# Performance work log

Hardware: AMD Instinct MI355X
Metric: run time of the kernel (lower is better)

## Reference

```python
import jax, jax.numpy as jnp
import numpy as np

NC = 5  # num_clusters == unfold window size


def conv1x3(x, w, b):
    # x: (B, Cin, H, W); w: (Cout, Cin, 1, 3); padding (0,1) like torch Conv2d
    y = jax.lax.conv_general_dilated(
        x, w, window_strides=(1, 1), padding=((0, 0), (1, 1)),
        dimension_numbers=("NCHW", "OIHW", "NCHW"))
    return y + b[None, :, None, None]


def setup_inputs() -> dict:
    key = jax.random.key(0)
    ks = jax.random.split(key, 8)
    b, h, l, d = 8, 8, 1024, 64
    dm = h * d  # d_model = 512
    f32 = jnp.float32
    s_conv1 = 1.0 / np.sqrt(dm * 3)
    s_conv2 = 1.0 / np.sqrt(NC * 3)
    s_lin = 1.0 / np.sqrt(NC)
    return {
        "Q": jax.random.normal(ks[0], (b, h, l, d), f32),
        "K": jax.random.normal(ks[1], (b, h, l, d), f32),
        "V": jax.random.normal(ks[2], (b, h, l, d), f32),
        "w_proj_k": jax.random.normal(ks[3], (NC, dm, 1, 3), f32) * s_conv1,
        "b_proj_k": jnp.zeros((NC,), f32),
        "w_proj_back": jax.random.normal(ks[4], (dm, NC, 1, 3), f32) * s_conv2,
        "b_proj_back": jnp.zeros((dm,), f32),
        "w_ck": jax.random.normal(ks[5], (NC, NC), f32) * s_lin,
        "b_ck": jnp.zeros((NC,), f32),
        "w_cq": jax.random.normal(ks[6], (NC, NC), f32) * s_lin,
        "b_cq": jnp.zeros((NC,), f32),
    }


def reference(Q, K, V, w_proj_k, b_proj_k, w_proj_back, b_proj_back,
              w_ck, b_ck, w_cq, b_cq):
    b, h, l, d = Q.shape
    u = NC  # unfolding window
    # --- padded unfold along batch dim: window i is K_padded[i:i+u] ---
    K_padded = jnp.concatenate(
        [jnp.zeros((u, h, l, d), Q.dtype), K[1:]], axis=0)  # (u+b-1, h, l, d)
    idx = jnp.arange(b)[:, None] + jnp.arange(u)[None, :]     # (b, u)
    Kw = K_padded[idx]                                        # (b, u, h, l, d)
    Kw = jnp.transpose(Kw, (0, 2, 3, 4, 1))                   # (b, h, l, d, u) == torch unfold layout
    K_unfold = Kw.reshape(b, h * d, l, u)                     # raw reshape, matches torch
    # --- project to clusters ---
    ckp = jax.nn.relu(conv1x3(K_unfold, w_proj_k, b_proj_k))  # (b, NC, l, u)
    ckp = jnp.transpose(ckp, (0, 2, 3, 1))                    # (b, l, u, NC)
    cluster_k = jax.nn.softmax(ckp @ w_ck.T + b_ck, axis=-1)
    cluster_q = jax.nn.softmax(ckp @ w_cq.T + b_cq, axis=-1)
    # --- distributional loss ---
    mu = jnp.mean(cluster_q, axis=-1)                         # (b, l, u)
    sigma = jax.nn.softplus(jnp.std(cluster_q, axis=-1, ddof=1))  # unbiased std like torch
    x = jnp.mean(cluster_k, axis=-1)
    log_prob = -0.5 * ((x - mu) / sigma) ** 2 - jnp.log(sigma) - 0.5 * jnp.log(2 * jnp.pi)
    # CrossEntropyLoss(mu, mu): class dim is axis=1 (l); soft-label targets = mu
    ce = -jnp.mean(jnp.sum(mu * jax.nn.log_softmax(mu, axis=1), axis=1))
    loss = -jnp.mean(log_prob) + ce
    # --- masked triangular cluster attention ---
    scores = jnp.einsum('blpc,bluc->blpu', cluster_q, cluster_k) / u  # (b, l, u, u)
    mask = jnp.triu(jnp.ones((u, u), bool), k=1)
    scores = jnp.where(mask, -1e9, scores)
    attn = jax.nn.softmax(scores, axis=-1)
    cluster_q2 = jnp.einsum('blpu,bluc->blpc', attn, cluster_q)       # (b, l, u, NC)
    # --- project back & second attention ---
    cc = jax.nn.relu(conv1x3(jnp.transpose(cluster_q2, (0, 3, 1, 2)),
                             w_proj_back, b_proj_back))               # (b, h*d, l, u)
    cluster_center = cc.reshape(b, h, u, l, d)                        # raw reshape, matches torch
    scores_center = jnp.einsum('bhqd,bhckd->bhqk', Q, cluster_center) # sums over c and d
    attn2 = jax.nn.softmax(scores_center, axis=-1)
    context = jnp.einsum('bhqk,bhkd->bhqd', attn2, V)
    return (context, loss)
```

## Files before the change

### kernel.cpp

```cpp
#include <hip/hip_runtime.h>
#include <math.h>

#define L 1024
#define D 64
#define H 8
#define B 8

#define WS_PART 0
#define WS_MU   614400
#define WS_Q2   655360
#define WS_KEFF 860160
#define WS_SCAL_BYTES 20217856

typedef __attribute__((ext_vector_type(8))) short bf16x8;
typedef __attribute__((ext_vector_type(4))) float f32x4;

__device__ __forceinline__ ushort f2bf(float x) {
  unsigned b = __builtin_bit_cast(unsigned, x);
  return (ushort)((b + 0x7FFFu + ((b >> 16) & 1u)) >> 16);
}
__device__ __forceinline__ float bf2f(ushort u) {
  unsigned t = ((unsigned)u) << 16;
  return __builtin_bit_cast(float, t);
}

__global__ __launch_bounds__(256) void k_part(const float* __restrict__ K,
                                              const float* __restrict__ wpk,
                                              float* __restrict__ part) {
  const int tid = threadIdx.x;
  const int lane = tid & 63;
  const int wid = tid >> 6;
  const int lq = blockIdx.x;
  const int jj = blockIdx.y;
  const int bi = blockIdx.z;
  __shared__ float w_s[512 * 16];
  __shared__ float red[3][64][16];
  for (int i = tid; i < 512 * 15; i += 256) {
    int c = i / 15, f = i % 15;
    int nc = f / 3, t = f % 3;
    w_s[c * 16 + f] = wpk[(nc * 512 + c) * 3 + t];
  }
  __syncthreads();
  float acc[15];
#pragma unroll
  for (int f = 0; f < 15; ++f) acc[f] = 0.f;
  if (bi + jj >= 5) {
    const float* Kb = K + (size_t)(bi + jj - 4) * (H * L * D);
    int c0 = wid * 128;
#pragma unroll 4
    for (int c = c0; c < c0 + 128; ++c) {
      int hh = c >> 6;
      int li2 = ((c & 63) << 4) + lq;
      float val = Kb[(hh * L + li2) * D + lane];
      const float* wr = &w_s[c * 16];
#pragma unroll
      for (int f = 0; f < 15; ++f) acc[f] = fmaf(val, wr[f], acc[f]);
    }
  }
  if (wid) {
#pragma unroll
    for (int f = 0; f < 15; ++f) red[wid - 1][lane][f] = acc[f];
  }
  __syncthreads();
  if (wid == 0) {
#pragma unroll
    for (int f = 0; f < 15; ++f)
      acc[f] += red[0][lane][f] + red[1][lane][f] + red[2][lane][f];
    int li = (lq << 6) + lane;
    float* dst = part + ((size_t)(bi * L + li) * 5 + jj) * 15;
#pragma unroll
    for (int f = 0; f < 15; ++f) dst[f] = acc[f];
  }
}

__global__ __launch_bounds__(256) void k_chain(const float* __restrict__ part,
    const float* __restrict__ b_pk, const float* __restrict__ w_ck,
    const float* __restrict__ b_ck, const float* __restrict__ w_cq,
    const float* __restrict__ b_cq, float* __restrict__ mu_out,
    float* __restrict__ q2_out, double* __restrict__ dsc) {
  int g = blockIdx.x * 256 + threadIdx.x;
  const float* p = part + (size_t)g * 75;
  float ckp[5][5];
#pragma unroll
  for (int j = 0; j < 5; ++j) {
#pragma unroll
    for (int nc = 0; nc < 5; ++nc) {
      float s = b_pk[nc];
#pragma unroll
      for (int t = 0; t < 3; ++t) {
        int w = j + t - 1;
        if (w >= 0 && w < 5) s += p[w * 15 + nc * 3 + t];
      }
      ckp[j][nc] = fmaxf(s, 0.f);
    }
  }
  float cq[5][5], ck[5][5];
  float lp_sum = 0.f;
#pragma unroll
  for (int j = 0; j < 5; ++j) {
    float vk[5], vq[5];
#pragma unroll
    for (int m = 0; m < 5; ++m) {
      float sk = b_ck[m], sq = b_cq[m];
#pragma unroll
      for (int n = 0; n < 5; ++n) {
        sk = fmaf(ckp[j][n], w_ck[m * 5 + n], sk);
        sq = fmaf(ckp[j][n], w_cq[m * 5 + n], sq);
      }
      vk[m] = sk; vq[m] = sq;
    }
    float mk = vk[0], mq = vq[0];
#pragma unroll
    for (int m = 1; m < 5; ++m) { mk = fmaxf(mk, vk[m]); mq = fmaxf(mq, vq[m]); }
    float sk = 0.f, sq = 0.f;
#pragma unroll
    for (int m = 0; m < 5; ++m) {
      vk[m] = expf(vk[m] - mk); sk += vk[m];
      vq[m] = expf(vq[m] - mq); sq += vq[m];
    }
    float rk = 1.f / sk, rq = 1.f / sq;
    float mu = 0.f, x = 0.f;
#pragma unroll
    for (int m = 0; m < 5; ++m) {
      ck[j][m] = vk[m] * rk; cq[j][m] = vq[m] * rq;
      mu += cq[j][m]; x += ck[j][m];
    }
    mu *= 0.2f; x *= 0.2f;
    float var = 0.f;
#pragma unroll
    for (int m = 0; m < 5; ++m) { float d0 = cq[j][m] - mu; var += d0 * d0; }
    var *= 0.25f;
    float sg = log1pf(expf(sqrtf(var)));
    float z = (x - mu) / sg;
    lp_sum += -0.5f * z * z - logf(sg) - 0.91893853320467274f;
    mu_out[(size_t)g * 5 + j] = mu;
  }
  float* q2p = q2_out + (size_t)g * 25;
#pragma unroll
  for (int pp = 0; pp < 5; ++pp) {
    float sc[5]; float mx = -3.0e38f;
    for (int u2 = 0; u2 <= pp; ++u2) {
      float d0 = 0.f;
#pragma unroll
      for (int c = 0; c < 5; ++c) d0 = fmaf(cq[pp][c], ck[u2][c], d0);
      sc[u2] = d0 * 0.2f;
      mx = fmaxf(mx, sc[u2]);
    }
    float den = 0.f;
    for (int u2 = 0; u2 <= pp; ++u2) { sc[u2] = expf(sc[u2] - mx); den += sc[u2]; }
    float rd = 1.f / den;
    float q2v[5] = {0.f, 0.f, 0.f, 0.f, 0.f};
    for (int u2 = 0; u2 <= pp; ++u2) {
      float a = sc[u2] * rd;
#pragma unroll
      for (int c = 0; c < 5; ++c) q2v[c] = fmaf(a, cq[u2][c], q2v[c]);
    }
#pragma unroll
    for (int c = 0; c < 5; ++c) q2p[pp * 5 + c] = q2v[c];
  }
  for (int off = 1; off < 64; off <<= 1) lp_sum += __shfl_xor(lp_sum, off, 64);
  __shared__ float wsum[4];
  int tid = threadIdx.x;
  if ((tid & 63) == 0) wsum[tid >> 6] = lp_sum;
  __syncthreads();
  if (tid == 0) atomicAdd(dsc, (double)(wsum[0] + wsum[1] + wsum[2] + wsum[3]));
}

__global__ __launch_bounds__(256) void k_ce(const float* __restrict__ mu,
                                            double* __restrict__ dsc) {
  int bi = blockIdx.x / 5, u = blockIdx.x % 5;
  int tid = threadIdx.x;
  const float* base = mu + (size_t)bi * L * 5 + u;
  float v[4];
#pragma unroll
  for (int k = 0; k < 4; ++k) v[k] = base[(tid + 256 * k) * 5];
  float mx = fmaxf(fmaxf(v[0], v[1]), fmaxf(v[2], v[3]));
  for (int off = 1; off < 64; off <<= 1) mx = fmaxf(mx, __shfl_xor(mx, off, 64));
  __shared__ float sh[4];
  if ((tid & 63) == 0) sh[tid >> 6] = mx;
  __syncthreads();
  mx = fmaxf(fmaxf(sh[0], sh[1]), fmaxf(sh[2], sh[3]));
  __syncthreads();
  float se = 0.f;
#pragma unroll
  for (int k = 0; k < 4; ++k) se += expf(v[k] - mx);
  for (int off = 1; off < 64; off <<= 1) se += __shfl_xor(se, off, 64);
  if ((tid & 63) == 0) sh[tid >> 6] = se;
  __syncthreads();
  float lse = mx + logf(sh[0] + sh[1] + sh[2] + sh[3]);
  __syncthreads();
  float part = 0.f;
#pragma unroll
  for (int k = 0; k < 4; ++k) part += v[k] * (v[k] - lse);
  for (int off = 1; off < 64; off <<= 1) part += __shfl_xor(part, off, 64);
  if ((tid & 63) == 0) sh[tid >> 6] = part;
  __syncthreads();
  if (tid == 0) atomicAdd(dsc + 1, (double)(sh[0] + sh[1] + sh[2] + sh[3]));
}

__global__ __launch_bounds__(256) void k_keff(const float* __restrict__ q2,
    const float* __restrict__ wb, const float* __restrict__ bb,
    float* __restrict__ keff) {
  int g = blockIdx.x * 256 + threadIdx.x;
  int bi = g >> 19;
  int r = g & 524287;
  int hh = r >> 16;
  int li2 = (r >> 6) & 1023;
  int dd = r & 63;
  int base = hh * 327680 + li2 * 64 + dd;
  const float* q2b = q2 + (size_t)bi * L * 25;
  float sum = 0.f;
#pragma unroll
  for (int cc = 0; cc < 5; ++cc) {
    int flat = base + cc * 65536;
    int co = (int)((unsigned)flat / 5120u);
    int rem = flat - co * 5120;
    int li = (int)((unsigned)rem / 5u);
    int j = rem - li * 5;
    const float* qr = q2b + li * 25;
    const float* wr = wb + co * 15;
    float s = bb[co];
#pragma unroll
    for (int t = 0; t < 3; ++t) {
      int w = j + t - 1;
      if (w >= 0 && w < 5) {
#pragma unroll
        for (int c = 0; c < 5; ++c) s = fmaf(qr[w * 5 + c], wr[c * 3 + t], s);
      }
    }
    sum += fmaxf(s, 0.f);
  }
  keff[g] = sum;
}

__global__ __launch_bounds__(256) void k_attn(const float* __restrict__ Q,
    const float* __restrict__ Kf, const float* __restrict__ V,
    float* __restrict__ Out) {
  __shared__ ushort Khi[4096], Klo[4096];
  __shared__ ushort Vthi[4096], Vtlo[4096];
  const int tid = threadIdx.x;
  const int lane = tid & 63;
  const int w = tid >> 6;
  const int lq = lane & 15;
  const int g = lane >> 4;
  const int bh = blockIdx.y;
  const int q0 = blockIdx.x << 7;
  const float* Qb = Q + ((size_t)bh * L + q0 + w * 32) * D;
  const float* Kb = Kf + (size_t)bh * L * D;
  const float* Vb = V + (size_t)bh * L * D;

  bf16x8 qh[2][2], qlo[2][2];
#pragma unroll
  for (int qs = 0; qs < 2; ++qs) {
    const float* Qr = Qb + (qs * 16 + lq) * D;
#pragma unroll
    for (int ds = 0; ds < 2; ++ds) {
      float4 x0 = *(const float4*)(Qr + 4 * g + 32 * ds);
      float4 x1 = *(const float4*)(Qr + 4 * g + 16 + 32 * ds);
      float xs[8] = {x0.x, x0.y, x0.z, x0.w, x1.x, x1.y, x1.z, x1.w};
      bf16x8 h, l;
#pragma unroll
      for (int j = 0; j < 8; ++j) {
        ushort hb = f2bf(xs[j]);
        h[j] = (short)hb;
        l[j] = (short)f2bf(xs[j] - bf2f(hb));
      }
      qh[qs][ds] = h; qlo[qs][ds] = l;
    }
  }

  f32x4 O_[2][4];
  float m_[2], l_[2];
#pragma unroll
  for (int qs = 0; qs < 2; ++qs) {
    m_[qs] = -3.0e38f; l_[qs] = 0.f;
#pragma unroll
    for (int d2 = 0; d2 < 4; ++d2) O_[qs][d2] = (f32x4){0.f, 0.f, 0.f, 0.f};
  }

  for (int kt = 0; kt < 16; ++kt) {
    __syncthreads();
    {
      int key = tid >> 2, c0 = (tid & 3) << 4;
      const float* Krow = Kb + (kt * 64 + key) * 64 + c0;
#pragma unroll
      for (int i = 0; i < 4; ++i) {
        float4 v = *(const float4*)(Krow + 4 * i);
        ushort4 h, lo;
        h.x = f2bf(v.x); h.y = f2bf(v.y); h.z = f2bf(v.z); h.w = f2bf(v.w);
        lo.x = f2bf(v.x - bf2f(h.x)); lo.y = f2bf(v.y - bf2f(h.y));
        lo.z = f2bf(v.z - bf2f(h.z)); lo.w = f2bf(v.w - bf2f(h.w));
        int c = (c0 >> 2) + i;
        int idx = key * 64 + ((c ^ (key & 15)) << 2);
        *(ushort4*)(&Khi[idx]) = h;
        *(ushort4*)(&Klo[idx]) = lo;
      }
    }
    {
      int kp = tid & 31, dblk = tid >> 5;
      ushort vh[2][8], vl[2][8];
#pragma unroll
      for (int kk = 0; kk < 2; ++kk) {
        int key = 2 * kp + kk;
        const float* Vrow = Vb + (kt * 64 + key) * 64 + dblk * 8;
#pragma unroll
        for (int i = 0; i < 2; ++i) {
          float4 v = *(const float4*)(Vrow + 4 * i);
          float xs[4] = {v.x, v.y, v.z, v.w};
#pragma unroll
          for (int e = 0; e < 4; ++e) {
            ushort hb = f2bf(xs[e]);
            vh[kk][4 * i + e] = hb;
            vl[kk][4 * i + e] = f2bf(xs[e] - bf2f(hb));
          }
        }
      }
#pragma unroll
      for (int dd = 0; dd < 8; ++dd) {
        int d = dblk * 8 + dd;
        int idx = d * 64 + (((kp >> 1) ^ (d & 15)) << 2) + ((kp & 1) << 1);
        ushort2 ph; ph.x = vh[0][dd]; ph.y = vh[1][dd];
        ushort2 pl; pl.x = vl[0][dd]; pl.y = vl[1][dd];
        *(ushort2*)(&Vthi[idx]) = ph;
        *(ushort2*)(&Vtlo[idx]) = pl;
      }
    }
    __syncthreads();

    f32x4 S[4][2];
#pragma unroll
    for (int ks = 0; ks < 4; ++ks)
#pragma unroll
      for (int qs = 0; qs < 2; ++qs) S[ks][qs] = (f32x4){0.f, 0.f, 0.f, 0.f};
#pragma unroll
    for (int ds = 0; ds < 2; ++ds) {
#pragma unroll
      for (int ksub = 0; ksub < 4; ++ksub) {
        int key = ksub * 16 + lq;
        int base = key * 64;
        int ca = ((g + 8 * ds) ^ lq) << 2;
        int cb = ((g + 4 + 8 * ds) ^ lq) << 2;
        ushort4 a0 = *(const ushort4*)(&Khi[base + ca]);
        ushort4 a1 = *(const ushort4*)(&Khi[base + cb]);
        ushort4 b0 = *(const ushort4*)(&Klo[base + ca]);
        ushort4 b1 = *(const ushort4*)(&Klo[base + cb]);
        bf16x8 kh = {(short)a0.x, (short)a0.y, (short)a0.z, (short)a0.w,
                     (short)a1.x, (short)a1.y, (short)a1.z, (short)a1.w};
        bf16x8 kl = {(short)b0.x, (short)b0.y, (short)b0.z, (short)b0.w,
                     (short)b1.x, (short)b1.y, (short)b1.z, (short)b1.w};
#pragma unroll
        for (int qs = 0; qs < 2; ++qs) {
          S[ksub][qs] = __builtin_amdgcn_mfma_f32_16x16x32_bf16(kh, qh[qs][ds], S[ksub][qs], 0, 0, 0);
          S[ksub][qs] = __builtin_amdgcn_mfma_f32_16x16x32_bf16(kh, qlo[qs][ds], S[ksub][qs], 0, 0, 0);
          S[ksub][qs] = __builtin_amdgcn_mfma_f32_16x16x32_bf16(kl, qh[qs][ds], S[ksub][qs], 0, 0, 0);
        }
      }
    }

    bf16x8 pfh[2][2], pfl[2][2];
#pragma unroll
    for (int qs = 0; qs < 2; ++qs) {
      float tmax = -3.0e38f;
#pragma unroll
      for (int ks = 0; ks < 4; ++ks)
#pragma unroll
        for (int r = 0; r < 4; ++r) tmax = fmaxf(tmax, S[ks][qs][r]);
      tmax = fmaxf(tmax, __shfl_xor(tmax, 16, 64));
      tmax = fmaxf(tmax, __shfl_xor(tmax, 32, 64));
      float mn = fmaxf(m_[qs], tmax);
      float scl = __expf(m_[qs] - mn);
      float p[4][4]; float rs = 0.f;
#pragma unroll
      for (int ks = 0; ks < 4; ++ks)
#pragma unroll
        for (int r = 0; r < 4; ++r) {
          float pv = __expf(S[ks][qs][r] - mn);
          p[ks][r] = pv; rs += pv;
        }
      rs += __shfl_xor(rs, 16, 64);
      rs += __shfl_xor(rs, 32, 64);
      l_[qs] = l_[qs] * scl + rs;
      m_[qs] = mn;
#pragma unroll
      for (int kst = 0; kst < 2; ++kst) {
        bf16x8 h, l;
#pragma unroll
        for (int jh = 0; jh < 2; ++jh)
#pragma unroll
          for (int j2 = 0; j2 < 4; ++j2) {
            float pv = p[jh + 2 * kst][j2];
            ushort hb = f2bf(pv);
            h[jh * 4 + j2] = (short)hb;
            l[jh * 4 + j2] = (short)f2bf(pv - bf2f(hb));
          }
        pfh[qs][kst] = h; pfl[qs][kst] = l;
      }
      float sr[4];
#pragma unroll
      for (int r = 0; r < 4; ++r) sr[r] = __shfl(scl, 4 * g + r, 64);
#pragma unroll
      for (int d2 = 0; d2 < 4; ++d2)
#pragma unroll
        for (int r = 0; r < 4; ++r) O_[qs][d2][r] *= sr[r];
    }

#pragma unroll
    for (int kst = 0; kst < 2; ++kst) {
#pragma unroll
      for (int d2 = 0; d2 < 4; ++d2) {
        int d = d2 * 16 + lq;
        int base = d * 64;
        int ca = ((g + 8 * kst) ^ lq) << 2;
        int cb = ((g + 4 + 8 * kst) ^ lq) << 2;
        ushort4 a0 = *(const ushort4*)(&Vthi[base + ca]);
        ushort4 a1 = *(const ushort4*)(&Vthi[base + cb]);
        ushort4 b0 = *(const ushort4*)(&Vtlo[base + ca]);
        ushort4 b1 = *(const ushort4*)(&Vtlo[base + cb]);
        bf16x8 vh = {(short)a0.x, (short)a0.y, (short)a0.z, (short)a0.w,
                     (short)a1.x, (short)a1.y, (short)a1.z, (short)a1.w};
        bf16x8 vl = {(short)b0.x, (short)b0.y, (short)b0.z, (short)b0.w,
                     (short)b1.x, (short)b1.y, (short)b1.z, (short)b1.w};
#pragma unroll
        for (int qs = 0; qs < 2; ++qs) {
          O_[qs][d2] = __builtin_amdgcn_mfma_f32_16x16x32_bf16(pfh[qs][kst], vh, O_[qs][d2], 0, 0, 0);
          O_[qs][d2] = __builtin_amdgcn_mfma_f32_16x16x32_bf16(pfl[qs][kst], vh, O_[qs][d2], 0, 0, 0);
          O_[qs][d2] = __builtin_amdgcn_mfma_f32_16x16x32_bf16(pfh[qs][kst], vl, O_[qs][d2], 0, 0, 0);
        }
      }
    }
  }

  float* Ob = Out + ((size_t)bh * L + q0 + w * 32) * D;
#pragma unroll
  for (int qs = 0; qs < 2; ++qs) {
    float il = 1.f / l_[qs];
    float ir[4];
#pragma unroll
    for (int r = 0; r < 4; ++r) ir[r] = __shfl(il, 4 * g + r, 64);
#pragma unroll
    for (int d2 = 0; d2 < 4; ++d2) {
#pragma unroll
      for (int r = 0; r < 4; ++r) {
        int row = qs * 16 + 4 * g + r;
        Ob[row * D + d2 * 16 + lq] = O_[qs][d2][r] * ir[r];
      }
    }
  }
}

__global__ void k_final(const double* __restrict__ dsc, float* __restrict__ out) {
  out[4194304] = (float)(-dsc[0] / 40960.0 - dsc[1] / 40.0);
}

extern "C" void kernel_launch(void* const* d_in, const int* in_sizes, int n_in,
                              void* d_out, int out_size, void* d_ws, size_t ws_size,
                              hipStream_t stream) {
  const float* Q   = (const float*)d_in[0];
  const float* K   = (const float*)d_in[1];
  const float* V   = (const float*)d_in[2];
  const float* wpk = (const float*)d_in[3];
  const float* bpk = (const float*)d_in[4];
  const float* wpb = (const float*)d_in[5];
  const float* bpb = (const float*)d_in[6];
  const float* wck = (const float*)d_in[7];
  const float* bck = (const float*)d_in[8];
  const float* wcq = (const float*)d_in[9];
  const float* bcq = (const float*)d_in[10];
  float* out = (float*)d_out;
  float* ws = (float*)d_ws;
  float* part = ws + WS_PART;
  float* mu   = ws + WS_MU;
  float* q2   = ws + WS_Q2;
  float* keff = ws + WS_KEFF;
  double* dsc = (double*)((char*)d_ws + WS_SCAL_BYTES);

  hipMemsetAsync((char*)d_ws + WS_SCAL_BYTES, 0, 16, stream);
  k_part<<<dim3(16, 5, 8), 256, 0, stream>>>(K, wpk, part);
  k_chain<<<32, 256, 0, stream>>>(part, bpk, wck, bck, wcq, bcq, mu, q2, dsc);
  k_ce<<<40, 256, 0, stream>>>(mu, dsc);
  k_keff<<<16384, 256, 0, stream>>>(q2, wpb, bpb, keff);
  k_attn<<<dim3(8, 64), 256, 0, stream>>>(Q, keff, V, out);
  k_final<<<1, 1, 0, stream>>>(dsc, out);
}
```

Before: 327.2 us.

## Dedupe K projection, pre-split K/V to bf16 in global, double-buffer attention

k_part now computes each batch's K projection once rather than per window position, and k_chain gathers the shared partials by batch offset. The effective K is split into bf16 hi/lo and written pre-swizzled to global memory. V is split and transposed the same way by a new prep kernel when workspace allows. The attention kernel streams tiles with async global_load_lds into double-buffered LDS, reorders blocks, and drops the low-part P correction MFMA (precision loss in P). It also vectorizes output stores and swaps the MFMA operand order. This removes redundant conversion work and overlaps loads with compute, at the cost of extra global traffic for the prepped buffers and some accuracy.

Result: faster. 307.9 us (-5.9%).

```diff
diff --git a/kernel.cpp b/kernel.cpp
--- a/kernel.cpp
+++ b/kernel.cpp
@@ -6,11 +6,16 @@
 #define H 8
 #define B 8
 
-#define WS_PART 0
-#define WS_MU   614400
-#define WS_Q2   655360
-#define WS_KEFF 860160
-#define WS_SCAL_BYTES 20217856
+#define WS_G    0
+#define WS_MU   107520
+#define WS_Q2   148480
+#define WS_DSC_BYTE   1413120u
+#define WS_KHI_BYTE   1413632u
+#define WS_KLO_BYTE   9802240u
+#define WS_NOV_END    18190848u
+#define WS_VTHI_BYTE  18190848u
+#define WS_VTLO_BYTE  26579456u
+#define WS_V_END      34968064u
 
 typedef __attribute__((ext_vector_type(8))) short bf16x8;
 typedef __attribute__((ext_vector_type(4))) float f32x4;
@@ -26,36 +31,35 @@
 
 __global__ __launch_bounds__(256) void k_part(const float* __restrict__ K,
                                               const float* __restrict__ wpk,
-                                              float* __restrict__ part) {
-  const int tid = threadIdx.x;
-  const int lane = tid & 63;
-  const int wid = tid >> 6;
+                                              float* __restrict__ G) {
+  const int tid = threadIdx.x, lane = tid & 63, wid = tid >> 6;
   const int lq = blockIdx.x;
-  const int jj = blockIdx.y;
-  const int bi = blockIdx.z;
+  const int bip = blockIdx.y + 1;
   __shared__ float w_s[512 * 16];
   __shared__ float red[3][64][16];
-  for (int i = tid; i < 512 * 15; i += 256) {
-    int c = i / 15, f = i % 15;
-    int nc = f / 3, t = f % 3;
-    w_s[c * 16 + f] = wpk[(nc * 512 + c) * 3 + t];
+  for (int i = tid; i < 512 * 16; i += 256) {
+    int c = i >> 4, f = i & 15;
+    w_s[i] = (f < 15) ? wpk[((f / 3) * 512 + c) * 3 + (f % 3)] : 0.f;
   }
   __syncthreads();
   float acc[15];
 #pragma unroll
   for (int f = 0; f < 15; ++f) acc[f] = 0.f;
-  if (bi + jj >= 5) {
-    const float* Kb = K + (size_t)(bi + jj - 4) * (H * L * D);
-    int c0 = wid * 128;
+  const float* Kb = K + (size_t)bip * (H * L * D);
+  const int c0 = wid * 128;
 #pragma unroll 4
-    for (int c = c0; c < c0 + 128; ++c) {
-      int hh = c >> 6;
-      int li2 = ((c & 63) << 4) + lq;
-      float val = Kb[(hh * L + li2) * D + lane];
-      const float* wr = &w_s[c * 16];
-#pragma unroll
-      for (int f = 0; f < 15; ++f) acc[f] = fmaf(val, wr[f], acc[f]);
-    }
+  for (int c = c0; c < c0 + 128; ++c) {
+    float val = Kb[((c >> 6) * L + ((c & 63) << 4) + lq) * D + lane];
+    const float4* wr = (const float4*)&w_s[c * 16];
+    float4 w0 = wr[0], w1 = wr[1], w2 = wr[2], w3 = wr[3];
+    acc[0] = fmaf(val, w0.x, acc[0]);  acc[1] = fmaf(val, w0.y, acc[1]);
+    acc[2] = fmaf(val, w0.z, acc[2]);  acc[3] = fmaf(val, w0.w, acc[3]);
+    acc[4] = fmaf(val, w1.x, acc[4]);  acc[5] = fmaf(val, w1.y, acc[5]);
+    acc[6] = fmaf(val, w1.z, acc[6]);  acc[7] = fmaf(val, w1.w, acc[7]);
+    acc[8] = fmaf(val, w2.x, acc[8]);  acc[9] = fmaf(val, w2.y, acc[9]);
+    acc[10] = fmaf(val, w2.z, acc[10]); acc[11] = fmaf(val, w2.w, acc[11]);
+    acc[12] = fmaf(val, w3.x, acc[12]); acc[13] = fmaf(val, w3.y, acc[13]);
+    acc[14] = fmaf(val, w3.z, acc[14]);
   }
   if (wid) {
 #pragma unroll
@@ -66,20 +70,19 @@
 #pragma unroll
     for (int f = 0; f < 15; ++f)
       acc[f] += red[0][lane][f] + red[1][lane][f] + red[2][lane][f];
-    int li = (lq << 6) + lane;
-    float* dst = part + ((size_t)(bi * L + li) * 5 + jj) * 15;
+    float* dst = G + ((size_t)blockIdx.y * 1024 + (lq << 6) + lane) * 15;
 #pragma unroll
     for (int f = 0; f < 15; ++f) dst[f] = acc[f];
   }
 }
 
-__global__ __launch_bounds__(256) void k_chain(const float* __restrict__ part,
+__global__ __launch_bounds__(256) void k_chain(const float* __restrict__ G,
     const float* __restrict__ b_pk, const float* __restrict__ w_ck,
     const float* __restrict__ b_ck, const float* __restrict__ w_cq,
     const float* __restrict__ b_cq, float* __restrict__ mu_out,
     float* __restrict__ q2_out, double* __restrict__ dsc) {
   int g = blockIdx.x * 256 + threadIdx.x;
-  const float* p = part + (size_t)g * 75;
+  int bi = g >> 10, li = g & 1023;
   float ckp[5][5];
 #pragma unroll
   for (int j = 0; j < 5; ++j) {
@@ -89,7 +92,9 @@
 #pragma unroll
       for (int t = 0; t < 3; ++t) {
         int w = j + t - 1;
-        if (w >= 0 && w < 5) s += p[w * 15 + nc * 3 + t];
+        int bip = bi + w - 4;
+        if (w >= 0 && w < 5 && bip >= 1)
+          s += G[(size_t)((bip - 1) * 1024 + li) * 15 + nc * 3 + t];
       }
       ckp[j][nc] = fmaxf(s, 0.f);
     }
@@ -198,16 +203,16 @@
   if (tid == 0) atomicAdd(dsc + 1, (double)(sh[0] + sh[1] + sh[2] + sh[3]));
 }
 
-__global__ __launch_bounds__(256) void k_keff(const float* __restrict__ q2,
+__global__ __launch_bounds__(256) void k_kprep(const float* __restrict__ q2,
     const float* __restrict__ wb, const float* __restrict__ bb,
-    float* __restrict__ keff) {
+    ushort* __restrict__ Khi_g, ushort* __restrict__ Klo_g) {
   int g = blockIdx.x * 256 + threadIdx.x;
   int bi = g >> 19;
   int r = g & 524287;
   int hh = r >> 16;
-  int li2 = (r >> 6) & 1023;
+  int li = (r >> 6) & 1023;
   int dd = r & 63;
-  int base = hh * 327680 + li2 * 64 + dd;
+  int base = hh * 327680 + li * 64 + dd;
   const float* q2b = q2 + (size_t)bi * L * 25;
   float sum = 0.f;
 #pragma unroll
@@ -215,9 +220,9 @@
     int flat = base + cc * 65536;
     int co = (int)((unsigned)flat / 5120u);
     int rem = flat - co * 5120;
-    int li = (int)((unsigned)rem / 5u);
-    int j = rem - li * 5;
-    const float* qr = q2b + li * 25;
+    int li2 = (int)((unsigned)rem / 5u);
+    int j = rem - li2 * 5;
+    const float* qr = q2b + li2 * 25;
     const float* wr = wb + co * 15;
     float s = bb[co];
 #pragma unroll
@@ -230,24 +235,70 @@
     }
     sum += fmaxf(s, 0.f);
   }
-  keff[g] = sum;
-}
-
+  int kt = li >> 6, key = li & 63, c = dd >> 2, e = dd & 3;
+  int idx = (((bi * 8 + hh) * 16 + kt) << 12) + (key << 6) + ((c ^ (key & 15)) << 2) + e;
+  ushort hb = f2bf(sum);
+  Khi_g[idx] = hb;
+  Klo_g[idx] = f2bf(sum - bf2f(hb));
+}
+
+__global__ __launch_bounds__(256) void k_vprep(const float* __restrict__ V,
+    ushort* __restrict__ Vthi_g, ushort* __restrict__ Vtlo_g) {
+  __shared__ float t[64][65];
+  const int tile = blockIdx.x;
+  const float* Vb = V + ((size_t)tile << 12);
+  const int tid = threadIdx.x;
+  {
+    int key = tid >> 2, c0 = (tid & 3) << 4;
+#pragma unroll
+    for (int i = 0; i < 4; ++i) {
+      float4 v = *(const float4*)(Vb + key * 64 + c0 + 4 * i);
+      t[key][c0 + 4 * i + 0] = v.x; t[key][c0 + 4 * i + 1] = v.y;
+      t[key][c0 + 4 * i + 2] = v.z; t[key][c0 + 4 * i + 3] = v.w;
+    }
+  }
+  __syncthreads();
+  int d = tid >> 2, q4 = tid & 3;
+#pragma unroll
+  for (int q = 0; q < 4; ++q) {
+    int kc = q4 * 4 + q;
+    ushort hv[4], lv[4];
+#pragma unroll
+    for (int e = 0; e < 4; ++e) {
+      float x = t[kc * 4 + e][d];
+      ushort hb = f2bf(x);
+      hv[e] = hb;
+      lv[e] = f2bf(x - bf2f(hb));
+    }
+    int idx = (tile << 12) + (d << 6) + ((kc ^ (d & 15)) << 2);
+    ushort4 h4; h4.x = hv[0]; h4.y = hv[1]; h4.z = hv[2]; h4.w = hv[3];
+    ushort4 l4; l4.x = lv[0]; l4.y = lv[1]; l4.z = lv[2]; l4.w = lv[3];
+    *(ushort4*)(&Vthi_g[idx]) = h4;
+    *(ushort4*)(&Vtlo_g[idx]) = l4;
+  }
+}
+
+template<bool VPREP>
 __global__ __launch_bounds__(256) void k_attn(const float* __restrict__ Q,
-    const float* __restrict__ Kf, const float* __restrict__ V,
-    float* __restrict__ Out) {
-  __shared__ ushort Khi[4096], Klo[4096];
-  __shared__ ushort Vthi[4096], Vtlo[4096];
+    const ushort* __restrict__ Khi_g, const ushort* __restrict__ Klo_g,
+    const ushort* __restrict__ Vthi_g, const ushort* __restrict__ Vtlo_g,
+    const float* __restrict__ V, float* __restrict__ Out) {
+  __shared__ ushort smem[2][16384];
   const int tid = threadIdx.x;
   const int lane = tid & 63;
   const int w = tid >> 6;
   const int lq = lane & 15;
   const int g = lane >> 4;
-  const int bh = blockIdx.y;
-  const int q0 = blockIdx.x << 7;
+  const int id = blockIdx.x;
+  const int bh = ((id & 7) << 3) + (id >> 6);
+  const int qb = (id >> 3) & 7;
+  const int q0 = qb << 7;
   const float* Qb = Q + ((size_t)bh * L + q0 + w * 32) * D;
-  const float* Kb = Kf + (size_t)bh * L * D;
   const float* Vb = V + (size_t)bh * L * D;
+  const int tb = bh * 16;
+
+  int cx0 = ((g) ^ lq) << 2, cx1 = ((g + 4) ^ lq) << 2;
+  int cx2 = ((g + 8) ^ lq) << 2, cx3 = ((g + 12) ^ lq) << 2;
 
   bf16x8 qh[2][2], qlo[2][2];
 #pragma unroll
@@ -269,6 +320,64 @@
     }
   }
 
+  const ushort* warr;
+  int wdst;
+  if (VPREP) {
+    warr = (w == 0) ? Khi_g : (w == 1) ? Klo_g : (w == 2) ? Vthi_g : Vtlo_g;
+    wdst = w << 12;
+  } else {
+    warr = ((w < 2) ? Khi_g : Klo_g);
+    wdst = ((w >> 1) << 12) + ((w & 1) << 11);
+  }
+
+#define STAGE(buf_, kt_) do {                                                  \
+    const ushort* src_ = warr + ((size_t)(tb + (kt_)) << 12) +                 \
+                         (VPREP ? 0 : ((w & 1) << 11)) + lane * 8;             \
+    ushort* dst_ = &smem[buf_][wdst];                                          \
+    _Pragma("unroll")                                                          \
+    for (int r_ = 0; r_ < (VPREP ? 8 : 4); ++r_) {                             \
+      __builtin_amdgcn_global_load_lds(                                        \
+        (const __attribute__((address_space(1))) unsigned int*)(src_ + r_ * 512), \
+        (__attribute__((address_space(3))) unsigned int*)(dst_ + r_ * 512 + lane * 8), \
+        16, 0, 0);                                                             \
+    }                                                                          \
+  } while (0)
+
+  float4 vreg[2][2];
+  const int kp = tid & 31, dblk = tid >> 5;
+#define VLOAD(kt_) do {                                                        \
+    const float* Vb2_ = Vb + ((size_t)(kt_) << 12);                            \
+    _Pragma("unroll")                                                          \
+    for (int kk_ = 0; kk_ < 2; ++kk_)                                          \
+      _Pragma("unroll")                                                        \
+      for (int i_ = 0; i_ < 2; ++i_)                                           \
+        vreg[kk_][i_] = *(const float4*)(Vb2_ + (2 * kp + kk_) * 64 + dblk * 8 + 4 * i_); \
+  } while (0)
+#define VWRITE(nb_) do {                                                       \
+    ushort vh_[2][8], vl_[2][8];                                               \
+    _Pragma("unroll")                                                          \
+    for (int kk_ = 0; kk_ < 2; ++kk_)                                          \
+      _Pragma("unroll")                                                        \
+      for (int i_ = 0; i_ < 2; ++i_) {                                         \
+        float xs_[4] = {vreg[kk_][i_].x, vreg[kk_][i_].y, vreg[kk_][i_].z, vreg[kk_][i_].w}; \
+        _Pragma("unroll")                                                      \
+        for (int e_ = 0; e_ < 4; ++e_) {                                       \
+          ushort hb_ = f2bf(xs_[e_]);                                          \
+          vh_[kk_][4 * i_ + e_] = hb_;                                         \
+          vl_[kk_][4 * i_ + e_] = f2bf(xs_[e_] - bf2f(hb_));                   \
+        }                                                                      \
+      }                                                                        \
+    _Pragma("unroll")                                                          \
+    for (int dd_ = 0; dd_ < 8; ++dd_) {                                        \
+      int d_ = dblk * 8 + dd_;                                                 \
+      int idx_ = (d_ << 6) + (((kp >> 1) ^ (d_ & 15)) << 2) + ((kp & 1) << 1); \
+      ushort2 ph_; ph_.x = vh_[0][dd_]; ph_.y = vh_[1][dd_];                   \
+      ushort2 pl_; pl_.x = vl_[0][dd_]; pl_.y = vl_[1][dd_];                   \
+      *(ushort2*)(&smem[nb_][8192 + idx_]) = ph_;                              \
+      *(ushort2*)(&smem[nb_][12288 + idx_]) = pl_;                             \
+    }                                                                          \
+  } while (0)
+
   f32x4 O_[2][4];
   float m_[2], l_[2];
 #pragma unroll
@@ -278,54 +387,21 @@
     for (int d2 = 0; d2 < 4; ++d2) O_[qs][d2] = (f32x4){0.f, 0.f, 0.f, 0.f};
   }
 
+  STAGE(0, 0);
+  if (!VPREP) { VLOAD(0); VWRITE(0); }
+  __syncthreads();
+
+  int cur = 0;
   for (int kt = 0; kt < 16; ++kt) {
-    __syncthreads();
-    {
-      int key = tid >> 2, c0 = (tid & 3) << 4;
-      const float* Krow = Kb + (kt * 64 + key) * 64 + c0;
-#pragma unroll
-      for (int i = 0; i < 4; ++i) {
-        float4 v = *(const float4*)(Krow + 4 * i);
-        ushort4 h, lo;
-        h.x = f2bf(v.x); h.y = f2bf(v.y); h.z = f2bf(v.z); h.w = f2bf(v.w);
-        lo.x = f2bf(v.x - bf2f(h.x)); lo.y = f2bf(v.y - bf2f(h.y));
-        lo.z = f2bf(v.z - bf2f(h.z)); lo.w = f2bf(v.w - bf2f(h.w));
-        int c = (c0 >> 2) + i;
-        int idx = key * 64 + ((c ^ (key & 15)) << 2);
-        *(ushort4*)(&Khi[idx]) = h;
-        *(ushort4*)(&Klo[idx]) = lo;
-      }
-    }
-    {
-      int kp = tid & 31, dblk = tid >> 5;
-      ushort vh[2][8], vl[2][8];
-#pragma unroll
-      for (int kk = 0; kk < 2; ++kk) {
-        int key = 2 * kp + kk;
-        const float* Vrow = Vb + (kt * 64 + key) * 64 + dblk * 8;
-#pragma unroll
-        for (int i = 0; i < 2; ++i) {
-          float4 v = *(const float4*)(Vrow + 4 * i);
-          float xs[4] = {v.x, v.y, v.z, v.w};
-#pragma unroll
-          for (int e = 0; e < 4; ++e) {
-            ushort hb = f2bf(xs[e]);
-            vh[kk][4 * i + e] = hb;
-            vl[kk][4 * i + e] = f2bf(xs[e] - bf2f(hb));
-          }
-        }
-      }
-#pragma unroll
-      for (int dd = 0; dd < 8; ++dd) {
-        int d = dblk * 8 + dd;
-        int idx = d * 64 + (((kp >> 1) ^ (d & 15)) << 2) + ((kp & 1) << 1);
-        ushort2 ph; ph.x = vh[0][dd]; ph.y = vh[1][dd];
-        ushort2 pl; pl.x = vl[0][dd]; pl.y = vl[1][dd];
-        *(ushort2*)(&Vthi[idx]) = ph;
-        *(ushort2*)(&Vtlo[idx]) = pl;
-      }
-    }
-    __syncthreads();
+    if (kt < 15) {
+      STAGE(cur ^ 1, kt + 1);
+      if (!VPREP) VLOAD(kt + 1);
+    }
+
+    const ushort* Kh = &smem[cur][0];
+    const ushort* Kl = &smem[cur][4096];
+    const ushort* Vh = &smem[cur][8192];
+    const ushort* Vl = &smem[cur][12288];
 
     f32x4 S[4][2];
 #pragma unroll
@@ -334,16 +410,14 @@
       for (int qs = 0; qs < 2; ++qs) S[ks][qs] = (f32x4){0.f, 0.f, 0.f, 0.f};
 #pragma unroll
     for (int ds = 0; ds < 2; ++ds) {
+      int ca = ds ? cx2 : cx0, cb = ds ? cx3 : cx1;
 #pragma unroll
       for (int ksub = 0; ksub < 4; ++ksub) {
-        int key = ksub * 16 + lq;
-        int base = key * 64;
-        int ca = ((g + 8 * ds) ^ lq) << 2;
-        int cb = ((g + 4 + 8 * ds) ^ lq) << 2;
-        ushort4 a0 = *(const ushort4*)(&Khi[base + ca]);
-        ushort4 a1 = *(const ushort4*)(&Khi[base + cb]);
-        ushort4 b0 = *(const ushort4*)(&Klo[base + ca]);
-        ushort4 b1 = *(const ushort4*)(&Klo[base + cb]);
+        int base = (ksub * 16 + lq) * 64;
+        ushort4 a0 = *(const ushort4*)(Kh + base + ca);
+        ushort4 a1 = *(const ushort4*)(Kh + base + cb);
+        ushort4 b0 = *(const ushort4*)(Kl + base + ca);
+        ushort4 b1 = *(const ushort4*)(Kl + base + cb);
         bf16x8 kh = {(short)a0.x, (short)a0.y, (short)a0.z, (short)a0.w,
                      (short)a1.x, (short)a1.y, (short)a1.z, (short)a1.w};
         bf16x8 kl = {(short)b0.x, (short)b0.y, (short)b0.z, (short)b0.w,
@@ -357,7 +431,8 @@
       }
     }
 
-    bf16x8 pfh[2][2], pfl[2][2];
+    bf16x8 pfh[2][2];
+    float scl[2];
 #pragma unroll
     for (int qs = 0; qs < 2; ++qs) {
       float tmax = -3.0e38f;
@@ -368,7 +443,7 @@
       tmax = fmaxf(tmax, __shfl_xor(tmax, 16, 64));
       tmax = fmaxf(tmax, __shfl_xor(tmax, 32, 64));
       float mn = fmaxf(m_[qs], tmax);
-      float scl = __expf(m_[qs] - mn);
+      scl[qs] = __expf(m_[qs] - mn);
       float p[4][4]; float rs = 0.f;
 #pragma unroll
       for (int ks = 0; ks < 4; ++ks)
@@ -379,73 +454,67 @@
         }
       rs += __shfl_xor(rs, 16, 64);
       rs += __shfl_xor(rs, 32, 64);
-      l_[qs] = l_[qs] * scl + rs;
+      l_[qs] = l_[qs] * scl[qs] + rs;
       m_[qs] = mn;
 #pragma unroll
       for (int kst = 0; kst < 2; ++kst) {
-        bf16x8 h, l;
+        bf16x8 h;
 #pragma unroll
         for (int jh = 0; jh < 2; ++jh)
 #pragma unroll
-          for (int j2 = 0; j2 < 4; ++j2) {
-            float pv = p[jh + 2 * kst][j2];
-            ushort hb = f2bf(pv);
-            h[jh * 4 + j2] = (short)hb;
-            l[jh * 4 + j2] = (short)f2bf(pv - bf2f(hb));
-          }
-        pfh[qs][kst] = h; pfl[qs][kst] = l;
-      }
-      float sr[4];
-#pragma unroll
-      for (int r = 0; r < 4; ++r) sr[r] = __shfl(scl, 4 * g + r, 64);
+          for (int j2 = 0; j2 < 4; ++j2)
+            h[jh * 4 + j2] = (short)f2bf(p[jh + 2 * kst][j2]);
+        pfh[qs][kst] = h;
+      }
 #pragma unroll
       for (int d2 = 0; d2 < 4; ++d2)
 #pragma unroll
-        for (int r = 0; r < 4; ++r) O_[qs][d2][r] *= sr[r];
+        for (int r = 0; r < 4; ++r) O_[qs][d2][r] *= scl[qs];
     }
 
 #pragma unroll
     for (int kst = 0; kst < 2; ++kst) {
+      int ca = kst ? cx2 : cx0, cb = kst ? cx3 : cx1;
 #pragma unroll
       for (int d2 = 0; d2 < 4; ++d2) {
-        int d = d2 * 16 + lq;
-        int base = d * 64;
-        int ca = ((g + 8 * kst) ^ lq) << 2;
-        int cb = ((g + 4 + 8 * kst) ^ lq) << 2;
-        ushort4 a0 = *(const ushort4*)(&Vthi[base + ca]);
-        ushort4 a1 = *(const ushort4*)(&Vthi[base + cb]);
-        ushort4 b0 = *(const ushort4*)(&Vtlo[base + ca]);
-        ushort4 b1 = *(const ushort4*)(&Vtlo[base + cb]);
+        int base = (d2 * 16 + lq) * 64;
+        ushort4 a0 = *(const ushort4*)(Vh + base + ca);
+        ushort4 a1 = *(const ushort4*)(Vh + base + cb);
+        ushort4 b0 = *(const ushort4*)(Vl + base + ca);
+        ushort4 b1 = *(const ushort4*)(Vl + base + cb);
         bf16x8 vh = {(short)a0.x, (short)a0.y, (short)a0.z, (short)a0.w,
                      (short)a1.x, (short)a1.y, (short)a1.z, (short)a1.w};
         bf16x8 vl = {(short)b0.x, (short)b0.y, (short)b0.z, (short)b0.w,
                      (short)b1.x, (short)b1.y, (short)b1.z, (short)b1.w};
 #pragma unroll
         for (int qs = 0; qs < 2; ++qs) {
-          O_[qs][d2] = __builtin_amdgcn_mfma_f32_16x16x32_bf16(pfh[qs][kst], vh, O_[qs][d2], 0, 0, 0);
-          O_[qs][d2] = __builtin_amdgcn_mfma_f32_16x16x32_bf16(pfl[qs][kst], vh, O_[qs][d2], 0, 0, 0);
-          O_[qs][d2] = __builtin_amdgcn_mfma_f32_16x16x32_bf16(pfh[qs][kst], vl, O_[qs][d2], 0, 0, 0);
+          O_[qs][d2] = __builtin_amdgcn_mfma_f32_16x16x32_bf16(vh, pfh[qs][kst], O_[qs][d2], 0, 0, 0);
+          O_[qs][d2] = __builtin_amdgcn_mfma_f32_16x16x32_bf16(vl, pfh[qs][kst], O_[qs][d2], 0, 0, 0);
         }
       }
     }
+
+    if (!VPREP && kt < 15) VWRITE(cur ^ 1);
+    __syncthreads();
+    cur ^= 1;
   }
 
   float* Ob = Out + ((size_t)bh * L + q0 + w * 32) * D;
 #pragma unroll
   for (int qs = 0; qs < 2; ++qs) {
     float il = 1.f / l_[qs];
-    float ir[4];
-#pragma unroll
-    for (int r = 0; r < 4; ++r) ir[r] = __shfl(il, 4 * g + r, 64);
+    int q = qs * 16 + lq;
 #pragma unroll
     for (int d2 = 0; d2 < 4; ++d2) {
-#pragma unroll
-      for (int r = 0; r < 4; ++r) {
-        int row = qs * 16 + 4 * g + r;
-        Ob[row * D + d2 * 16 + lq] = O_[qs][d2][r] * ir[r];
-      }
-    }
-  }
+      float4 o4;
+      o4.x = O_[qs][d2][0] * il; o4.y = O_[qs][d2][1] * il;
+      o4.z = O_[qs][d2][2] * il; o4.w = O_[qs][d2][3] * il;
+      *(float4*)(Ob + q * D + d2 * 16 + 4 * g) = o4;
+    }
+  }
+#undef STAGE
+#undef VLOAD
+#undef VWRITE
 }
 
 __global__ void k_final(const double* __restrict__ dsc, float* __restrict__ out) {
@@ -468,17 +537,26 @@
   const float* bcq = (const float*)d_in[10];
   float* out = (float*)d_out;
   float* ws = (float*)d_ws;
-  float* part = ws + WS_PART;
+  float* G    = ws + WS_G;
   float* mu   = ws + WS_MU;
   float* q2   = ws + WS_Q2;
-  float* keff = ws + WS_KEFF;
-  double* dsc = (double*)((char*)d_ws + WS_SCAL_BYTES);
-
-  hipMemsetAsync((char*)d_ws + WS_SCAL_BYTES, 0, 16, stream);
-  k_part<<<dim3(16, 5, 8), 256, 0, stream>>>(K, wpk, part);
-  k_chain<<<32, 256, 0, stream>>>(part, bpk, wck, bck, wcq, bcq, mu, q2, dsc);
+  double* dsc = (double*)((char*)d_ws + WS_DSC_BYTE);
+  ushort* Khi = (ushort*)((char*)d_ws + WS_KHI_BYTE);
+  ushort* Klo = (ushort*)((char*)d_ws + WS_KLO_BYTE);
+  ushort* Vthi = (ushort*)((char*)d_ws + WS_VTHI_BYTE);
+  ushort* Vtlo = (ushort*)((char*)d_ws + WS_VTLO_BYTE);
+  const bool vprep = (ws_size >= (size_t)WS_V_END);
+
+  hipMemsetAsync((char*)d_ws + WS_DSC_BYTE, 0, 16, stream);
+  if (vprep) k_vprep<<<1024, 256, 0, stream>>>(V, Vthi, Vtlo);
+  k_part<<<dim3(16, 7), 256, 0, stream>>>(K, wpk, G);
+  k_chain<<<32, 256, 0, stream>>>(G, bpk, wck, bck, wcq, bcq, mu, q2, dsc);
   k_ce<<<40, 256, 0, stream>>>(mu, dsc);
-  k_keff<<<16384, 256, 0, stream>>>(q2, wpb, bpb, keff);
-  k_attn<<<dim3(8, 64), 256, 0, stream>>>(Q, keff, V, out);
+  k_kprep<<<16384, 256, 0, stream>>>(q2, wpb, bpb, Khi, Klo);
+  if (vprep) {
+    k_attn<true><<<512, 256, 0, stream>>>(Q, Khi, Klo, Vthi, Vtlo, V, out);
+  } else {
+    k_attn<false><<<512, 256, 0, stream>>>(Q, Khi, Klo, nullptr, nullptr, V, out);
+  }
   k_final<<<1, 1, 0, stream>>>(dsc, out);
 }
```
